# Optimization experiments

Measured on AMD Instinct MI355X. Metric: run time of the kernel, lower is better.

The kernel has to match this reference:

```python
import jax, jax.numpy as jnp
import numpy as np

KS = 3                      # kernel side
GRID_SIZE = 5
SPLINE_ORDER = 3
N_CONVS = 8
IN_FEAT = KS * KS           # KANLinear in_features per patch
NCOEF = GRID_SIZE + SPLINE_ORDER  # number of B-spline basis functions


def setup_inputs() -> dict:
    key = jax.random.key(0)
    k1, k2, k3, k4 = jax.random.split(key, 4)
    x = jax.random.normal(k1, (8, 32, 64, 64), jnp.float32)
    # efficient-kan KANLinear params, stacked over the n_convs independent kernels
    base_weight = jax.random.normal(k2, (N_CONVS, IN_FEAT), jnp.float32) / np.sqrt(IN_FEAT).astype(np.float32)
    spline_weight = jax.random.normal(k3, (N_CONVS, IN_FEAT, NCOEF), jnp.float32) * 0.1
    spline_scaler = jax.random.normal(k4, (N_CONVS, IN_FEAT), jnp.float32) / np.sqrt(IN_FEAT).astype(np.float32)
    # knot grid: uniform over grid_range=[-1,1], extended by spline_order on each side
    h = 2.0 / GRID_SIZE
    g = jnp.arange(-SPLINE_ORDER, GRID_SIZE + SPLINE_ORDER + 1, dtype=jnp.float32) * h - 1.0
    grid = jnp.tile(g[None, :], (IN_FEAT, 1))  # [in, G+2k+1]
    return {"x": x, "base_weight": base_weight, "spline_weight": spline_weight,
            "spline_scaler": spline_scaler, "grid": grid}


def b_splines(x, grid):
    # x: [..., in], grid: [in, G+2k+1] -> bases [..., in, G+k]  (Cox-de Boor)
    xe = x[..., None]
    bases = ((xe >= grid[:, :-1]) & (xe < grid[:, 1:])).astype(x.dtype)
    for k in range(1, SPLINE_ORDER + 1):
        left = (xe - grid[:, :-(k + 1)]) / (grid[:, k:-1] - grid[:, :-(k + 1)])
        right = (grid[:, k + 1:] - xe) / (grid[:, k + 1:] - grid[:, 1:-k])
        bases = left * bases[..., :-1] + right * bases[..., 1:]
    return bases


def reference(x, base_weight, spline_weight, spline_scaler, grid):
    B, C, H, W = x.shape
    ho, wo = H - KS + 1, W - KS + 1  # stride 1, dilation 1, no padding
    # im2col: [B, C*KS*KS, ho, wo], channel-major feature order (matches torch Unfold)
    patches = jax.lax.conv_general_dilated_patches(x, (KS, KS), (1, 1), 'VALID')
    patches = patches.reshape(B, C, IN_FEAT, ho * wo).transpose(0, 1, 3, 2)  # [B,C,L,in]
    # KANLinear(out_features=1) applied per conv n over each patch
    base = jnp.einsum('bcli,ni->bcnl', jax.nn.silu(patches), base_weight)
    basis = b_splines(patches, grid)                     # [B,C,L,in,coef]
    sw = spline_weight * spline_scaler[..., None]        # scaled spline weight [n,in,coef]
    spl = jnp.einsum('bclis,nis->bcnl', basis, sw)
    # output channel index = kern + channel * n_convs (channel-major)
    return (base + spl).reshape(B, C * N_CONVS, ho, wo)
```

## Files before the change

### kernel.cpp

```cpp
#include <hip/hip_runtime.h>
#include <hip/hip_bf16.h>


#define N_CONVS 8
#define HH 64
#define WW 64
#define HO 62
#define WO 62
#define BAND 8
#define LROWS 10
#define PW 66
#define PLANE (LROWS * PW)

__global__ __launch_bounds__(768) void kan_prep(const float* __restrict__ bw,
                                                const float* __restrict__ sw,
                                                const float* __restrict__ sc,
                                                float* __restrict__ wf) {
    const int t   = threadIdx.x;
    const int blk = t >> 5;
    const int r   = t & 31;
    const int ky  = blk >> 3, n = blk & 7;
    const int kx  = r / 10, j = r % 10;
    float v = 0.0f;
    if (kx < 3 && j <= 8) {
        const int i = ky * 3 + kx;
        v = (j == 0) ? bw[n * 9 + i]
                     : sw[(n * 9 + i) * 8 + (j - 1)] * sc[n * 9 + i];
    }
    wf[t] = v;
}

__global__ __launch_bounds__(256, 5) void kan_main(
    const float* __restrict__ x,
    const float* __restrict__ grid,
    const float* __restrict__ wf,
    float* __restrict__ out)
{
    __shared__ __align__(16) float feat[9 * PLANE];

    const int blk  = blockIdx.x;
    const int band = blk & 7;
    const int img  = blk >> 3;
    const int r0   = band * BAND;
    const int nr   = (HO - r0) < BAND  ? (HO - r0) : BAND;
    const int nin  = (HH - r0) < LROWS ? (HH - r0) : LROWS;

    const float g0   = grid[0];
    const float invh = __builtin_amdgcn_rcpf(grid[1] - grid[0]);

    const float* xb = x + (size_t)img * (HH * WW) + (size_t)r0 * WW;
    for (int p = threadIdx.x; p < nin * WW; p += 256) {
        const int r = p >> 6, c = p & 63;
        const float xv = xb[p];

        float* fp = &feat[r * PW + c];
        fp[0] = xv * __builtin_amdgcn_rcpf(1.0f + __expf(-xv));
#pragma unroll
        for (int j = 1; j < 9; j++) fp[j * PLANE] = 0.0f;

        const float u0 = (xv - g0) * invh;
        const int   m  = (int)floorf(u0);
        if (m >= 0 && m <= 10) {
            const float u  = u0 - (float)m;
            const float um = 1.0f - u;
            const float u2 = u * u, u3 = u2 * u;
            const float N0 = um * um * um * (1.0f / 6.0f);
            const float N1 = (3.0f * u3 - 6.0f * u2 + 4.0f) * (1.0f / 6.0f);
            const float N2 = (-3.0f * u3 + 3.0f * u2 + 3.0f * u + 1.0f) * (1.0f / 6.0f);
            const float N3 = u3 * (1.0f / 6.0f);
            const float Nv[4] = {N0, N1, N2, N3};
#pragma unroll
            for (int s = 0; s < 4; s++) {
                const int j = m - 3 + s;
                if (j >= 0 && j <= 7) fp[(j + 1) * PLANE] = Nv[s];
            }
        }
    }
    __syncthreads();

    const int row = threadIdx.x >> 5;
    const int xs  = (threadIdx.x & 31) << 1;
    if (row < nr && xs < WO) {
        float acc[N_CONVS][2];
#pragma unroll
        for (int n = 0; n < N_CONVS; n++) { acc[n][0] = 0.0f; acc[n][1] = 0.0f; }

#pragma unroll 1
        for (int ky = 0; ky < 3; ky++) {
            float fw[9][4];
#pragma unroll
            for (int j = 0; j < 9; j++) {
                const float* pl = &feat[j * PLANE + (row + ky) * PW + xs];
                const float2 a = *(const float2*)pl;
                const float2 b = *(const float2*)(pl + 2);
                fw[j][0] = a.x; fw[j][1] = a.y; fw[j][2] = b.x; fw[j][3] = b.y;
            }
            const float* wk = wf + (ky << 8);
#pragma unroll
            for (int n = 0; n < N_CONVS; n++) {
                const float* wn = wk + (n << 5);
#pragma unroll
                for (int kx = 0; kx < 3; kx++) {
                    const float* gg = wn + kx * 10;
#pragma unroll
                    for (int t = 0; t < 2; t++) {
                        float a = acc[n][t];
#pragma unroll
                        for (int j = 0; j < 9; j++)
                            a = fmaf(gg[j], fw[j][kx + t], a);
                        acc[n][t] = a;
                    }
                }
            }
        }

        const int oy = r0 + row;
        float* ob = out + (size_t)img * N_CONVS * (HO * WO) + oy * WO + xs;
#pragma unroll
        for (int n = 0; n < N_CONVS; n++)
            *(float2*)(ob + n * (HO * WO)) = make_float2(acc[n][0], acc[n][1]);
    }
}

extern "C" void kernel_launch(void* const* d_in, const int* in_sizes, int n_in,
                              void* d_out, int out_size, void* d_ws, size_t ws_size,
                              hipStream_t stream) {
    const float* x    = (const float*)d_in[0];
    const float* bw   = (const float*)d_in[1];
    const float* sw   = (const float*)d_in[2];
    const float* sc   = (const float*)d_in[3];
    const float* grid = (const float*)d_in[4];
    float* out = (float*)d_out;
    float* wf  = (float*)d_ws;

    kan_prep<<<1, 768, 0, stream>>>(bw, sw, sc, wf);
    kan_main<<<256 * 8, 256, 0, stream>>>(x, grid, wf, out);
}
```

Measured before the change: 87.56 us.

## Store spline feature planes in fp16 LDS and reorder weight layout per feature

Feature planes in shared memory change from fp32 to fp16, halving LDS use. The launch-bound occupancy hint rises from 5 to 8 blocks per CU. The weight table is re-laid out so each (ky, feature) chunk holds 24 contiguous weights, letting the inner loop consume one feature at a time instead of holding all 9x4 values in registers. The compute loop now runs for all threads, with only the store guarded. fp16 storage reduces precision of silu and basis values, and out-of-range threads read uninitialized padding LDS but discard the result.

```diff
diff --git a/kernel.cpp b/kernel.cpp
--- a/kernel.cpp
+++ b/kernel.cpp
@@ -12,17 +12,19 @@
 #define PW 66
 #define PLANE (LROWS * PW)
 
-__global__ __launch_bounds__(768) void kan_prep(const float* __restrict__ bw,
+typedef _Float16 half2v __attribute__((ext_vector_type(2)));
+
+__global__ __launch_bounds__(864) void kan_prep(const float* __restrict__ bw,
                                                 const float* __restrict__ sw,
                                                 const float* __restrict__ sc,
                                                 float* __restrict__ wf) {
-    const int t   = threadIdx.x;
-    const int blk = t >> 5;
-    const int r   = t & 31;
-    const int ky  = blk >> 3, n = blk & 7;
-    const int kx  = r / 10, j = r % 10;
+    const int t = threadIdx.x;
+    const int chunk = t >> 5;
+    const int r = t & 31;
+    const int ky = chunk / 9, j = chunk % 9;
     float v = 0.0f;
-    if (kx < 3 && j <= 8) {
+    if (r < 24) {
+        const int n = r / 3, kx = r % 3;
         const int i = ky * 3 + kx;
         v = (j == 0) ? bw[n * 9 + i]
                      : sw[(n * 9 + i) * 8 + (j - 1)] * sc[n * 9 + i];
@@ -30,13 +32,13 @@
     wf[t] = v;
 }
 
-__global__ __launch_bounds__(256, 5) void kan_main(
+__global__ __launch_bounds__(256, 8) void kan_main(
     const float* __restrict__ x,
     const float* __restrict__ grid,
     const float* __restrict__ wf,
     float* __restrict__ out)
 {
-    __shared__ __align__(16) float feat[9 * PLANE];
+    __shared__ _Float16 feat[9 * PLANE];
 
     const int blk  = blockIdx.x;
     const int band = blk & 7;
@@ -53,10 +55,10 @@
         const int r = p >> 6, c = p & 63;
         const float xv = xb[p];
 
-        float* fp = &feat[r * PW + c];
-        fp[0] = xv * __builtin_amdgcn_rcpf(1.0f + __expf(-xv));
+        _Float16* fp = &feat[r * PW + c];
+        fp[0] = (_Float16)(xv * __builtin_amdgcn_rcpf(1.0f + __expf(-xv)));
 #pragma unroll
-        for (int j = 1; j < 9; j++) fp[j * PLANE] = 0.0f;
+        for (int j = 1; j < 9; j++) fp[j * PLANE] = (_Float16)0.0f;
 
         const float u0 = (xv - g0) * invh;
         const int   m  = (int)floorf(u0);
@@ -72,7 +74,7 @@
 #pragma unroll
             for (int s = 0; s < 4; s++) {
                 const int j = m - 3 + s;
-                if (j >= 0 && j <= 7) fp[(j + 1) * PLANE] = Nv[s];
+                if (j >= 0 && j <= 7) fp[(j + 1) * PLANE] = (_Float16)Nv[s];
             }
         }
     }
@@ -80,40 +82,33 @@
 
     const int row = threadIdx.x >> 5;
     const int xs  = (threadIdx.x & 31) << 1;
-    if (row < nr && xs < WO) {
-        float acc[N_CONVS][2];
+
+    float acc[N_CONVS][2];
 #pragma unroll
-        for (int n = 0; n < N_CONVS; n++) { acc[n][0] = 0.0f; acc[n][1] = 0.0f; }
+    for (int n = 0; n < N_CONVS; n++) { acc[n][0] = 0.0f; acc[n][1] = 0.0f; }
 
 #pragma unroll 1
-        for (int ky = 0; ky < 3; ky++) {
-            float fw[9][4];
+    for (int ky = 0; ky < 3; ky++) {
 #pragma unroll
-            for (int j = 0; j < 9; j++) {
-                const float* pl = &feat[j * PLANE + (row + ky) * PW + xs];
-                const float2 a = *(const float2*)pl;
-                const float2 b = *(const float2*)(pl + 2);
-                fw[j][0] = a.x; fw[j][1] = a.y; fw[j][2] = b.x; fw[j][3] = b.y;
-            }
-            const float* wk = wf + (ky << 8);
+        for (int j = 0; j < 9; j++) {
+            const _Float16* pl = &feat[j * PLANE + (row + ky) * PW + xs];
+            const half2v a = *(const half2v*)pl;
+            const half2v b = *(const half2v*)(pl + 2);
+            const float fv[4] = {(float)a.x, (float)a.y, (float)b.x, (float)b.y};
+            const float* gg = wf + ((ky * 9 + j) << 5);
 #pragma unroll
             for (int n = 0; n < N_CONVS; n++) {
-                const float* wn = wk + (n << 5);
 #pragma unroll
                 for (int kx = 0; kx < 3; kx++) {
-                    const float* gg = wn + kx * 10;
-#pragma unroll
-                    for (int t = 0; t < 2; t++) {
-                        float a = acc[n][t];
-#pragma unroll
-                        for (int j = 0; j < 9; j++)
-                            a = fmaf(gg[j], fw[j][kx + t], a);
-                        acc[n][t] = a;
-                    }
+                    const float w = gg[n * 3 + kx];
+                    acc[n][0] = fmaf(w, fv[kx],     acc[n][0]);
+                    acc[n][1] = fmaf(w, fv[kx + 1], acc[n][1]);
                 }
             }
         }
+    }
 
+    if (row < nr && xs < WO) {
         const int oy = r0 + row;
         float* ob = out + (size_t)img * N_CONVS * (HO * WO) + oy * WO + xs;
 #pragma unroll
@@ -133,6 +128,6 @@
     float* out = (float*)d_out;
     float* wf  = (float*)d_ws;
 
-    kan_prep<<<1, 768, 0, stream>>>(bw, sw, sc, wf);
+    kan_prep<<<1, 864, 0, stream>>>(bw, sw, sc, wf);
     kan_main<<<256 * 8, 256, 0, stream>>>(x, grid, wf, out);
 }
```

Result: slower. 89.34 us (+2.0%).

## Fuse weight prep into main kernel and unroll feature staging loop

Applied to the files above, without the earlier changes.

Drops the separate prep kernel launch. The main kernel now reads base, spline and scaler weights directly and applies the scaler after summing the spline terms. The feature-staging loop is unrolled into three fixed loads per thread so global loads can be issued early. The compute loop now runs on every thread, with only the store guarded, and the occupancy hint rises from 5 to 6 blocks per SIMD. The trade is extra scalar weight loads and FMAs per block, plus higher register pressure.

```diff
diff --git a/kernel.cpp b/kernel.cpp
--- a/kernel.cpp
+++ b/kernel.cpp
@@ -12,28 +12,37 @@
 #define PW 66
 #define PLANE (LROWS * PW)
 
-__global__ __launch_bounds__(768) void kan_prep(const float* __restrict__ bw,
-                                                const float* __restrict__ sw,
-                                                const float* __restrict__ sc,
-                                                float* __restrict__ wf) {
-    const int t   = threadIdx.x;
-    const int blk = t >> 5;
-    const int r   = t & 31;
-    const int ky  = blk >> 3, n = blk & 7;
-    const int kx  = r / 10, j = r % 10;
-    float v = 0.0f;
-    if (kx < 3 && j <= 8) {
-        const int i = ky * 3 + kx;
-        v = (j == 0) ? bw[n * 9 + i]
-                     : sw[(n * 9 + i) * 8 + (j - 1)] * sc[n * 9 + i];
+__device__ __forceinline__ void compute_features(float xv, float g0, float invh,
+                                                 float* fp) {
+    fp[0] = xv * __builtin_amdgcn_rcpf(1.0f + __expf(-xv));
+#pragma unroll
+    for (int j = 1; j < 9; j++) fp[j * PLANE] = 0.0f;
+
+    const float u0 = (xv - g0) * invh;
+    const int   m  = (int)floorf(u0);
+    if (m >= 0 && m <= 10) {
+        const float u  = u0 - (float)m;
+        const float um = 1.0f - u;
+        const float u2 = u * u, u3 = u2 * u;
+        const float N0 = um * um * um * (1.0f / 6.0f);
+        const float N1 = (3.0f * u3 - 6.0f * u2 + 4.0f) * (1.0f / 6.0f);
+        const float N2 = (-3.0f * u3 + 3.0f * u2 + 3.0f * u + 1.0f) * (1.0f / 6.0f);
+        const float N3 = u3 * (1.0f / 6.0f);
+        const float Nv[4] = {N0, N1, N2, N3};
+#pragma unroll
+        for (int s = 0; s < 4; s++) {
+            const int j = m - 3 + s;
+            if (j >= 0 && j <= 7) fp[(j + 1) * PLANE] = Nv[s];
+        }
     }
-    wf[t] = v;
 }
 
-__global__ __launch_bounds__(256, 5) void kan_main(
+__global__ __launch_bounds__(256, 6) void kan_main(
     const float* __restrict__ x,
+    const float* __restrict__ bw,
+    const float* __restrict__ sw,
+    const float* __restrict__ sc,
     const float* __restrict__ grid,
-    const float* __restrict__ wf,
     float* __restrict__ out)
 {
     __shared__ __align__(16) float feat[9 * PLANE];
@@ -44,76 +53,70 @@
     const int r0   = band * BAND;
     const int nr   = (HO - r0) < BAND  ? (HO - r0) : BAND;
     const int nin  = (HH - r0) < LROWS ? (HH - r0) : LROWS;
+    const int npix = nin * WW;
 
     const float g0   = grid[0];
     const float invh = __builtin_amdgcn_rcpf(grid[1] - grid[0]);
 
+    const int t = threadIdx.x;
     const float* xb = x + (size_t)img * (HH * WW) + (size_t)r0 * WW;
-    for (int p = threadIdx.x; p < nin * WW; p += 256) {
-        const int r = p >> 6, c = p & 63;
-        const float xv = xb[p];
+    const float xv0 = xb[t];
+    const float xv1 = xb[t + 256];
+    const bool  has2 = (t + 512 < npix);
+    float xv2 = 0.0f;
+    if (has2) xv2 = xb[t + 512];
 
-        float* fp = &feat[r * PW + c];
-        fp[0] = xv * __builtin_amdgcn_rcpf(1.0f + __expf(-xv));
-#pragma unroll
-        for (int j = 1; j < 9; j++) fp[j * PLANE] = 0.0f;
-
-        const float u0 = (xv - g0) * invh;
-        const int   m  = (int)floorf(u0);
-        if (m >= 0 && m <= 10) {
-            const float u  = u0 - (float)m;
-            const float um = 1.0f - u;
-            const float u2 = u * u, u3 = u2 * u;
-            const float N0 = um * um * um * (1.0f / 6.0f);
-            const float N1 = (3.0f * u3 - 6.0f * u2 + 4.0f) * (1.0f / 6.0f);
-            const float N2 = (-3.0f * u3 + 3.0f * u2 + 3.0f * u + 1.0f) * (1.0f / 6.0f);
-            const float N3 = u3 * (1.0f / 6.0f);
-            const float Nv[4] = {N0, N1, N2, N3};
-#pragma unroll
-            for (int s = 0; s < 4; s++) {
-                const int j = m - 3 + s;
-                if (j >= 0 && j <= 7) fp[(j + 1) * PLANE] = Nv[s];
-            }
-        }
+    compute_features(xv0, g0, invh, &feat[(t >> 6) * PW + (t & 63)]);
+    {
+        const int p = t + 256;
+        compute_features(xv1, g0, invh, &feat[(p >> 6) * PW + (p & 63)]);
+    }
+    if (has2) {
+        const int p = t + 512;
+        compute_features(xv2, g0, invh, &feat[(p >> 6) * PW + (p & 63)]);
     }
     __syncthreads();
 
     const int row = threadIdx.x >> 5;
     const int xs  = (threadIdx.x & 31) << 1;
-    if (row < nr && xs < WO) {
-        float acc[N_CONVS][2];
+
+    float acc[N_CONVS][2];
 #pragma unroll
-        for (int n = 0; n < N_CONVS; n++) { acc[n][0] = 0.0f; acc[n][1] = 0.0f; }
+    for (int n = 0; n < N_CONVS; n++) { acc[n][0] = 0.0f; acc[n][1] = 0.0f; }
 
 #pragma unroll 1
-        for (int ky = 0; ky < 3; ky++) {
-            float fw[9][4];
+    for (int ky = 0; ky < 3; ky++) {
+        float fw[9][4];
 #pragma unroll
-            for (int j = 0; j < 9; j++) {
-                const float* pl = &feat[j * PLANE + (row + ky) * PW + xs];
-                const float2 a = *(const float2*)pl;
-                const float2 b = *(const float2*)(pl + 2);
-                fw[j][0] = a.x; fw[j][1] = a.y; fw[j][2] = b.x; fw[j][3] = b.y;
-            }
-            const float* wk = wf + (ky << 8);
+        for (int j = 0; j < 9; j++) {
+            const float* pl = &feat[j * PLANE + (row + ky) * PW + xs];
+            const float2 a = *(const float2*)pl;
+            const float2 b = *(const float2*)(pl + 2);
+            fw[j][0] = a.x; fw[j][1] = a.y; fw[j][2] = b.x; fw[j][3] = b.y;
+        }
 #pragma unroll
-            for (int n = 0; n < N_CONVS; n++) {
-                const float* wn = wk + (n << 5);
+        for (int n = 0; n < N_CONVS; n++) {
+            const float* swp = sw + (n * 9 + ky * 3) * 8;
+            const float* bwp = bw + n * 9 + ky * 3;
+            const float* scp = sc + n * 9 + ky * 3;
 #pragma unroll
-                for (int kx = 0; kx < 3; kx++) {
-                    const float* gg = wn + kx * 10;
+            for (int kx = 0; kx < 3; kx++) {
+                float s0 = 0.0f, s1 = 0.0f;
 #pragma unroll
-                    for (int t = 0; t < 2; t++) {
-                        float a = acc[n][t];
-#pragma unroll
-                        for (int j = 0; j < 9; j++)
-                            a = fmaf(gg[j], fw[j][kx + t], a);
-                        acc[n][t] = a;
-                    }
+                for (int j = 0; j < 8; j++) {
+                    const float w = swp[kx * 8 + j];
+                    s0 = fmaf(w, fw[j + 1][kx],     s0);
+                    s1 = fmaf(w, fw[j + 1][kx + 1], s1);
                 }
+                acc[n][0] = fmaf(scp[kx], s0, acc[n][0]);
+                acc[n][1] = fmaf(scp[kx], s1, acc[n][1]);
+                acc[n][0] = fmaf(bwp[kx], fw[0][kx],     acc[n][0]);
+                acc[n][1] = fmaf(bwp[kx], fw[0][kx + 1], acc[n][1]);
             }
         }
+    }
 
+    if (row < nr && xs < WO) {
         const int oy = r0 + row;
         float* ob = out + (size_t)img * N_CONVS * (HO * WO) + oy * WO + xs;
 #pragma unroll
@@ -131,8 +134,6 @@
     const float* sc   = (const float*)d_in[3];
     const float* grid = (const float*)d_in[4];
     float* out = (float*)d_out;
-    float* wf  = (float*)d_ws;
 
-    kan_prep<<<1, 768, 0, stream>>>(bw, sw, sc, wf);
-    kan_main<<<256 * 8, 256, 0, stream>>>(x, grid, wf, out);
+    kan_main<<<256 * 8, 256, 0, stream>>>(x, bw, sw, sc, grid, out);
 }
```

New measurement: 112.7 us. +28.7%, slower.
